# Kernel optimization log

Measured on AMD Instinct MI355X. Metric: run time of the kernel, lower is better.

The kernel has to match this reference:

```python
import jax, jax.numpy as jnp
import numpy as np

LOG_SIG_MIN, LOG_SIG_MAX = -20.0, 2.0
BN_EPS = 1e-5

def leaky_relu(x):
    return jnp.where(x >= 0, x, 0.01 * x)

def setup_inputs() -> dict:
    key = jax.random.key(0)
    ks = jax.random.split(key, 12)
    E, B, N, H, A = 8, 16384, 64, 512, 8  # encoders, batch, nagents, hidden, heads
    d = H // A
    f32 = jnp.float32
    inp = {}
    inp['states'] = jax.random.normal(ks[0], (E, B, N), dtype=f32)
    inp['pre_actions'] = jax.random.normal(ks[1], (B, H), dtype=f32)
    inp['W_enc'] = jax.random.normal(ks[2], (E, N, H), dtype=f32) / np.sqrt(N)
    inp['b_enc'] = jnp.zeros((E, H), dtype=f32)
    inp['W_pre'] = jax.random.normal(ks[3], (H, H), dtype=f32) / np.sqrt(H)
    inp['b_pre'] = jnp.zeros((H,), dtype=f32)
    inp['Wk'] = jax.random.normal(ks[4], (A, H, d), dtype=f32) / np.sqrt(H)
    inp['Wsel'] = jax.random.normal(ks[5], (A, H, d), dtype=f32) / np.sqrt(H)
    inp['Wv'] = jax.random.normal(ks[6], (A, H, d), dtype=f32) / np.sqrt(H)
    inp['bv'] = jnp.zeros((A, d), dtype=f32)
    inp['W_actor'] = jax.random.normal(ks[7], (H, H), dtype=f32) / np.sqrt(H)
    inp['b_actor'] = jnp.zeros((H,), dtype=f32)
    inp['W_mean'] = jax.random.normal(ks[8], (H, N), dtype=f32) / np.sqrt(H)
    inp['b_mean'] = jnp.zeros((N,), dtype=f32)
    inp['W_logstd'] = jax.random.normal(ks[9], (H, N), dtype=f32) / np.sqrt(H)
    inp['b_logstd'] = jnp.zeros((N,), dtype=f32)
    return inp

def reference(states, pre_actions, W_enc, b_enc, W_pre, b_pre, Wk, Wsel, Wv, bv,
              W_actor, b_actor, W_mean, b_mean, W_logstd, b_logstd):
    # states: [E, B, N]; per-encoder BatchNorm1d (training-mode batch stats, no affine)
    mu = states.mean(axis=1, keepdims=True)                      # [E,1,N]
    var = states.var(axis=1, keepdims=True)                      # biased var, as torch BN
    s_norm = (states - mu) * jax.lax.rsqrt(var + BN_EPS)
    # per-encoder Linear + LeakyReLU -> encodings [E, B, H]
    encs = leaky_relu(jnp.einsum('ebn,enh->ebh', s_norm, W_enc) + b_enc[:, None, :])
    # per-head keys/values over all encoders: [A, E, B, d]
    keys = jnp.einsum('ebh,ahd->aebd', encs, Wk)
    vals = leaky_relu(jnp.einsum('ebh,ahd->aebd', encs, Wv) + bv[:, None, None, :])
    # selector from encoded previous actions: [A, B, d]
    pre = leaky_relu(pre_actions @ W_pre + b_pre)                 # [B, H]
    sel = jnp.einsum('bh,ahd->abd', pre, Wsel)
    d = keys.shape[-1]
    logits = jnp.einsum('abd,aebd->abe', sel, keys)               # [A, B, E]
    w = jax.nn.softmax(logits / np.sqrt(d), axis=-1)
    attn = jnp.einsum('aebd,abe->abd', vals, w)                   # [A, B, d]
    B = attn.shape[1]
    actor_in = jnp.transpose(attn, (1, 0, 2)).reshape(B, -1)      # [B, A*d] head-concat
    x = jax.nn.relu(actor_in @ W_actor + b_actor)
    mean = x @ W_mean + b_mean
    log_std = jnp.clip(x @ W_logstd + b_logstd, LOG_SIG_MIN, LOG_SIG_MAX)
    return mean, log_std, actor_in
```

## Files before the change

kernel.cpp:

```cpp
#include <hip/hip_runtime.h>
#include <hip/hip_bf16.h>
#include <stdint.h>

#define E_ 8
#define B_ 16384
#define N_ 64
#define H_ 512
#define A_ 8
#define D_ 64

typedef __hip_bfloat16 bf16;
typedef __attribute__((ext_vector_type(8))) short s8v;
typedef __attribute__((ext_vector_type(4))) float f4v;

__device__ __forceinline__ float bf2f(bf16 v) { return __bfloat162float(v); }
__device__ __forceinline__ bf16 f2bf(float v) { return __float2bfloat16(v); }
__device__ __forceinline__ short f2bfs(float v) {
    bf16 b = f2bf(v); short s; __builtin_memcpy(&s, &b, 2); return s;
}
__device__ __forceinline__ float bfs2f(short s) {
    bf16 b; __builtin_memcpy(&b, &s, 2); return bf2f(b);
}

__device__ __forceinline__ void async_load16(const void* g, void* l) {
    __builtin_amdgcn_global_load_lds(
        (const __attribute__((address_space(1))) void*)g,
        (__attribute__((address_space(3))) void*)l, 16, 0, 0);
}

__device__ __forceinline__ int swz_off(int row, int krow) {
    return row * 64 + (((krow >> 3) ^ (row & 7)) << 3);
}

template <int CB>
__device__ __forceinline__ void xcd_map(int x, int nBm, int& bm, int& bn) {
    if ((nBm & 7) == 0) {
        int j = x & 7, s = x >> 3;
        bn = s & ((1 << CB) - 1);
        bm = ((s >> CB) << 3) | j;
    } else {
        bm = x >> CB;
        bn = x & ((1 << CB) - 1);
    }
}

__global__ __launch_bounds__(256) void bnPart(const float* __restrict__ states,
                                              float* __restrict__ part,
                                              bf16* __restrict__ sbf) {
    int blk = blockIdx.x;
    int e = blk >> 6, sl = blk & 63;
    int tid = threadIdx.x, n = tid & 63, rg = tid >> 6;
    const long rowBase = (long)e * B_ + (long)sl * 256;
    const float* base = states + rowBase * 64;
    float s1 = 0.f, s2 = 0.f;
    for (int i = 0; i < 64; ++i) {
        float v = base[(rg + i * 4) * 64 + n];
        s1 += v; s2 += v * v;
        sbf[(rowBase + rg + i * 4) * 64 + n] = f2bf(v);
    }
    __shared__ float sh[2][4][64];
    sh[0][rg][n] = s1; sh[1][rg][n] = s2;
    __syncthreads();
    if (tid < 64) {
        float t1 = sh[0][0][n] + sh[0][1][n] + sh[0][2][n] + sh[0][3][n];
        float t2 = sh[1][0][n] + sh[1][1][n] + sh[1][2][n] + sh[1][3][n];
        part[((long)blk * 64 + n) * 2 + 0] = t1;
        part[((long)blk * 64 + n) * 2 + 1] = t2;
    }
}

__global__ void bnFin(const float* __restrict__ part, float* __restrict__ mu_rstd) {
    int idx = blockIdx.x * blockDim.x + threadIdx.x;
    if (idx >= E_ * 64) return;
    int e = idx >> 6, n = idx & 63;
    float s1 = 0.f, s2 = 0.f;
    for (int sl = 0; sl < 64; ++sl) {
        s1 += part[(((long)e * 64 + sl) * 64 + n) * 2 + 0];
        s2 += part[(((long)e * 64 + sl) * 64 + n) * 2 + 1];
    }
    float mu = s1 / (float)B_;
    float var = s2 / (float)B_ - mu * mu;
    mu_rstd[idx * 2 + 0] = mu;
    mu_rstd[idx * 2 + 1] = rsqrtf(var + 1e-5f);
}

__global__ void foldEnc(const float* __restrict__ W_enc, const float* __restrict__ b_enc,
                        const float* __restrict__ mu_rstd,
                        bf16* __restrict__ WencfT, float* __restrict__ bencf) {
    int idx = blockIdx.x * 256 + threadIdx.x;
    int e = idx >> 9, h = idx & 511;
    float acc = b_enc[e * 512 + h];
    for (int n = 0; n < 64; ++n) {
        float mu = mu_rstd[(e * 64 + n) * 2 + 0];
        float rs = mu_rstd[(e * 64 + n) * 2 + 1];
        float w = W_enc[((long)e * 64 + n) * 512 + h];
        WencfT[((long)e * 512 + h) * 64 + n] = f2bf(w * rs);
        acc -= mu * rs * w;
    }
    bencf[e * 512 + h] = acc;
}

__global__ __launch_bounds__(256) void packAll(
    const float* __restrict__ W_pre, const float* __restrict__ W_actor,
    const float* __restrict__ Wsel, const float* __restrict__ Wk,
    const float* __restrict__ Wv, const float* __restrict__ wm,
    const float* __restrict__ wl, const float* __restrict__ pre_actions,
    bf16* __restrict__ WpreT, bf16* __restrict__ WactorT, bf16* __restrict__ WselT,
    bf16* __restrict__ WkvaT, bf16* __restrict__ WmlT, bf16* __restrict__ pa_bf) {
    int bx = blockIdx.x, tid = threadIdx.x;
    if (bx < 2048) {
        const float* in = (bx < 1024) ? W_pre : W_actor;
        bf16* out = (bx < 1024) ? WpreT : WactorT;
        int idx = (bx & 1023) * 256 + tid;
        int n = idx >> 9, k = idx & 511;
        out[idx] = f2bf(in[k * 512 + n]);
    } else if (bx < 3072) {
        int idx = (bx - 2048) * 256 + tid;
        int n = idx >> 9, h = idx & 511;
        int a = n >> 6, dd = n & 63;
        WselT[idx] = f2bf(Wsel[((long)a * 512 + h) * 64 + dd]);
    } else if (bx < 5120) {
        int idx = (bx - 3072) * 256 + tid;
        int n = idx >> 9, h = idx & 511;
        int a = n >> 7, j = n & 127;
        const float* src = (j < 64) ? Wk : Wv;
        WkvaT[idx] = f2bf(src[((long)a * 512 + h) * 64 + (j & 63)]);
    } else if (bx < 5376) {
        int idx = (bx - 5120) * 256 + tid;
        int n = idx >> 9, k = idx & 511;
        float v = (n < 64) ? wm[k * 64 + n] : wl[k * 64 + (n - 64)];
        WmlT[idx] = f2bf(v);
    } else {
        int i = (bx - 5376) * 256 + tid;
        float4 v = ((const float4*)pre_actions)[i];
        bf16 o[4] = {f2bf(v.x), f2bf(v.y), f2bf(v.z), f2bf(v.w)};
        __builtin_memcpy(pa_bf + (long)i * 4, o, 8);
    }
}

template <int ACT, int OUTF, bool HAS_BIAS, int CB>
__global__ __launch_bounds__(256) void gemm_bt(
    const bf16* __restrict__ Ag, const bf16* __restrict__ Bg,
    const float* __restrict__ bias, const float* __restrict__ bias2,
    void* __restrict__ out, void* __restrict__ out2,
    int M, int Nn, int K, long sA, long sB, long sBias, long sO) {
    const int tid = threadIdx.x, lane = tid & 63, wid = tid >> 6;
    const int wm = wid >> 1, wn = wid & 1;
    int bm, bn;
    xcd_map<CB>(blockIdx.x, gridDim.x >> CB, bm, bn);
    const int bz = blockIdx.z;
    const bf16* Aptr = Ag + (long)bz * sA + (long)bm * 128 * K;
    const bf16* Bptr = Bg + (long)bz * sB + (long)bn * 128 * K;

    __shared__ __align__(16) short sAl[128 * 64];
    __shared__ __align__(16) short sBl[128 * 64];

    const int srow = lane >> 3;
    const int scol = (((lane & 7) ^ srow) << 3);

    f4v acc[4][4];
#pragma unroll
    for (int i = 0; i < 4; ++i)
#pragma unroll
        for (int j = 0; j < 4; ++j) acc[i][j] = f4v{0.f, 0.f, 0.f, 0.f};

    for (int k0 = 0; k0 < K; k0 += 64) {
#pragma unroll
        for (int i = 0; i < 4; ++i) {
            int r = (wid * 4 + i) * 8 + srow;
            async_load16(Aptr + (long)r * K + k0 + scol, (char*)sAl + (wid * 4 + i) * 1024);
            async_load16(Bptr + (long)r * K + k0 + scol, (char*)sBl + (wid * 4 + i) * 1024);
        }
        __syncthreads();
#pragma unroll
        for (int kk = 0; kk < 64; kk += 32) {
            int krow = kk + (lane >> 4) * 8;
            s8v af[4], bfr[4];
#pragma unroll
            for (int mi = 0; mi < 4; ++mi)
                af[mi] = *(const s8v*)(sAl + swz_off(wm * 64 + mi * 16 + (lane & 15), krow));
#pragma unroll
            for (int ni = 0; ni < 4; ++ni)
                bfr[ni] = *(const s8v*)(sBl + swz_off(wn * 64 + ni * 16 + (lane & 15), krow));
#pragma unroll
            for (int mi = 0; mi < 4; ++mi)
#pragma unroll
                for (int ni = 0; ni < 4; ++ni)
                    acc[mi][ni] = __builtin_amdgcn_mfma_f32_16x16x32_bf16(
                        af[mi], bfr[ni], acc[mi][ni], 0, 0, 0);
        }
        __syncthreads();
    }

    long m0 = (long)bm * 128 + wm * 64;
    long n0 = (long)bn * 128 + wn * 64;
#pragma unroll
    for (int mi = 0; mi < 4; ++mi)
#pragma unroll
        for (int ni = 0; ni < 4; ++ni)
#pragma unroll
            for (int r = 0; r < 4; ++r) {
                long gm = m0 + mi * 16 + (lane >> 4) * 4 + r;
                long gn = n0 + ni * 16 + (lane & 15);
                float v = acc[mi][ni][r];
                if constexpr (HAS_BIAS) v += bias[sBias * bz + gn];
                if constexpr (ACT == 1) v = (v >= 0.f) ? v : 0.01f * v;
                if constexpr (ACT == 2) v = fmaxf(v, 0.f);
                if constexpr (OUTF == 0) {
                    ((bf16*)out)[(long)bz * sO + gm * Nn + gn] = f2bf(v);
                } else if constexpr (OUTF == 1) {
                    ((float*)out)[(long)bz * sO + gm * Nn + gn] = v;
                } else if constexpr (OUTF == 2) {
                    if (gn < 64) {
                        ((float*)out)[gm * 64 + gn] = v + bias[gn];
                    } else {
                        float w = v + bias2[gn - 64];
                        w = fminf(fmaxf(w, -20.f), 2.f);
                        ((float*)out2)[gm * 64 + (gn - 64)] = w;
                    }
                } else {
                    ((bf16*)out)[(gm * E_ + bz) * 512 + gn] = f2bf(v);
                }
            }
}

__global__ __launch_bounds__(256) void kv_attn(
    const bf16* __restrict__ Ag, const bf16* __restrict__ Bg,
    const float* __restrict__ bv, const float* __restrict__ sel,
    float* __restrict__ actor_f32, bf16* __restrict__ attn_bf, int b0) {
    const int tid = threadIdx.x, lane = tid & 63, wid = tid >> 6;
    const int wm = wid >> 1, wn = wid & 1;
    int bm, a;
    xcd_map<3>(blockIdx.x, gridDim.x >> 3, bm, a);
    const bf16* Aptr = Ag + (long)bm * 128 * 512;
    const bf16* Bptr = Bg + (long)a * 128 * 512;

    __shared__ __align__(16) short smem[17408];
    __shared__ float lgs[128];
    short* sAl = smem;
    short* sBl = smem + 128 * 64;

    const long bgBase = (long)b0 + (long)bm * 16;

    s8v bselH[2], bselL[2];
#pragma unroll
    for (int kk = 0; kk < 2; ++kk) {
        const float* sp = sel + (bgBase + (lane & 15)) * 512 + a * 64 + kk * 32 + (lane >> 4) * 8;
#pragma unroll
        for (int j = 0; j < 8; ++j) {
            float s = sp[j] * 0.125f;
            short h = f2bfs(s);
            bselH[kk][j] = h;
            bselL[kk][j] = f2bfs(s - bfs2f(h));
        }
    }

    const int srow = lane >> 3;
    const int scol = (((lane & 7) ^ srow) << 3);

    f4v acc[4][4];
#pragma unroll
    for (int i = 0; i < 4; ++i)
#pragma unroll
        for (int j = 0; j < 4; ++j) acc[i][j] = f4v{0.f, 0.f, 0.f, 0.f};

    for (int k0 = 0; k0 < 512; k0 += 64) {
#pragma unroll
        for (int i = 0; i < 4; ++i) {
            int r = (wid * 4 + i) * 8 + srow;
            async_load16(Aptr + (long)r * 512 + k0 + scol, (char*)sAl + (wid * 4 + i) * 1024);
            async_load16(Bptr + (long)r * 512 + k0 + scol, (char*)sBl + (wid * 4 + i) * 1024);
        }
        __syncthreads();
#pragma unroll
        for (int kk = 0; kk < 64; kk += 32) {
            int krow = kk + (lane >> 4) * 8;
            s8v af[4], bfr[4];
#pragma unroll
            for (int mi = 0; mi < 4; ++mi)
                af[mi] = *(const s8v*)(sAl + swz_off(wm * 64 + mi * 16 + (lane & 15), krow));
#pragma unroll
            for (int ni = 0; ni < 4; ++ni)
                bfr[ni] = *(const s8v*)(sBl + swz_off(wn * 64 + ni * 16 + (lane & 15), krow));
#pragma unroll
            for (int mi = 0; mi < 4; ++mi)
#pragma unroll
                for (int ni = 0; ni < 4; ++ni)
                    acc[mi][ni] = __builtin_amdgcn_mfma_f32_16x16x32_bf16(
                        af[mi], bfr[ni], acc[mi][ni], 0, 0, 0);
        }
        __syncthreads();
    }

    short* keysC = smem;
    short* vT    = smem + 9216;
    const int quad = lane >> 4, cl = lane & 15;
#pragma unroll
    for (int mi = 0; mi < 4; ++mi)
#pragma unroll
        for (int ni = 0; ni < 4; ++ni)
#pragma unroll
            for (int r = 0; r < 4; ++r) {
                int row = wm * 64 + mi * 16 + quad * 4 + r;
                float v = acc[mi][ni][r];
                if (wn == 0) {
                    keysC[row * 72 + ni * 16 + cl] = f2bfs(v);
                } else {
                    int d = ni * 16 + cl;
                    v += bv[a * 64 + d];
                    v = (v >= 0.f) ? v : 0.01f * v;
                    vT[d * 128 + (row ^ ((d & 15) << 3))] = f2bfs(v);
                }
            }
    __syncthreads();

    {
        f4v lgacc[2] = {f4v{0.f, 0.f, 0.f, 0.f}, f4v{0.f, 0.f, 0.f, 0.f}};
#pragma unroll
        for (int kk = 0; kk < 2; ++kk) {
#pragma unroll
            for (int mi = 0; mi < 2; ++mi) {
                s8v af = *(const s8v*)(keysC + (wid * 32 + mi * 16 + cl) * 72 +
                                       kk * 32 + quad * 8);
                lgacc[mi] = __builtin_amdgcn_mfma_f32_16x16x32_bf16(
                    af, bselH[kk], lgacc[mi], 0, 0, 0);
                lgacc[mi] = __builtin_amdgcn_mfma_f32_16x16x32_bf16(
                    af, bselL[kk], lgacc[mi], 0, 0, 0);
            }
        }
#pragma unroll
        for (int mi = 0; mi < 2; ++mi)
#pragma unroll
            for (int r = 0; r < 4; ++r) {
                int grow = wid * 32 + mi * 16 + quad * 4 + r;
                if (cl == (grow >> 3)) lgs[grow] = lgacc[mi][r];
            }
    }
    __syncthreads();

#pragma unroll
    for (int t = 0; t < 4; ++t) {
        int lb = wid * 4 + t, row0 = lb * 8;
        s8v vvv = *(const s8v*)(vT + lane * 128 + (row0 ^ ((lane & 15) << 3)));
        float lg[8], vv[8];
#pragma unroll
        for (int e = 0; e < 8; ++e) {
            vv[e] = bfs2f(vvv[e]);
            lg[e] = lgs[row0 + e];
        }
        float mx = lg[0];
#pragma unroll
        for (int e = 1; e < 8; ++e) mx = fmaxf(mx, lg[e]);
        float ssum = 0.f, w[8];
#pragma unroll
        for (int e = 0; e < 8; ++e) { w[e] = __expf(lg[e] - mx); ssum += w[e]; }
        float inv = 1.f / ssum;
        float at = 0.f;
#pragma unroll
        for (int e = 0; e < 8; ++e) at += vv[e] * (w[e] * inv);
        long o = (bgBase + lb) * 512 + a * 64 + lane;
        actor_f32[o] = at;
        attn_bf[o] = f2bf(at);
    }
}

extern "C" void kernel_launch(void* const* d_in, const int* in_sizes, int n_in,
                              void* d_out, int out_size, void* d_ws, size_t ws_size,
                              hipStream_t stream) {
    (void)in_sizes; (void)n_in; (void)out_size;
    const float* states      = (const float*)d_in[0];
    const float* pre_actions = (const float*)d_in[1];
    const float* W_enc       = (const float*)d_in[2];
    const float* b_enc       = (const float*)d_in[3];
    const float* W_pre       = (const float*)d_in[4];
    const float* b_pre       = (const float*)d_in[5];
    const float* Wk          = (const float*)d_in[6];
    const float* Wsel        = (const float*)d_in[7];
    const float* Wv          = (const float*)d_in[8];
    const float* bv          = (const float*)d_in[9];
    const float* W_actor     = (const float*)d_in[10];
    const float* b_actor     = (const float*)d_in[11];
    const float* W_mean      = (const float*)d_in[12];
    const float* b_mean      = (const float*)d_in[13];
    const float* W_logstd    = (const float*)d_in[14];
    const float* b_logstd    = (const float*)d_in[15];

    char* ws = (char*)d_ws;
    size_t off = 0;
    auto alloc = [&](size_t bytes) -> void* {
        void* p = ws + off;
        off = (off + bytes + 255) & ~(size_t)255;
        return p;
    };
    float* mu_rstd = (float*)alloc((size_t)E_ * 64 * 2 * 4);
    float* bnpart  = (float*)alloc((size_t)E_ * 64 * 64 * 2 * 4);
    bf16* WencfT   = (bf16*)alloc((size_t)E_ * 512 * 64 * 2);
    float* bencf   = (float*)alloc((size_t)E_ * 512 * 4);
    bf16* WpreT    = (bf16*)alloc((size_t)512 * 512 * 2);
    bf16* WselT    = (bf16*)alloc((size_t)512 * 512 * 2);
    bf16* WkvaT    = (bf16*)alloc((size_t)1024 * 512 * 2);
    bf16* WactorT  = (bf16*)alloc((size_t)512 * 512 * 2);
    bf16* WmlT     = (bf16*)alloc((size_t)128 * 512 * 2);
    bf16* pa_bf    = (bf16*)alloc((size_t)B_ * 512 * 2);
    bf16* p_pre    = (bf16*)alloc((size_t)B_ * 512 * 2);
    float* p_sel   = (float*)alloc((size_t)B_ * 512 * 4);
    bf16* s_bf     = (bf16*)alloc((size_t)E_ * B_ * 64 * 2);
    bf16* p_attn = pa_bf;
    bf16* p_x    = p_pre;

    size_t remaining = (ws_size > off) ? ws_size - off : 0;
    int Bc = B_;
    while (Bc > 128 && (size_t)Bc * 8192 + 4096 > remaining) Bc >>= 1;
    const int NC = B_ / Bc;
    bf16* c_encs = (bf16*)alloc((size_t)E_ * Bc * 512 * 2);

    packAll<<<13568, 256, 0, stream>>>(W_pre, W_actor, Wsel, Wk, Wv, W_mean, W_logstd,
                                       pre_actions, WpreT, WactorT, WselT, WkvaT, WmlT,
                                       pa_bf);
    bnPart<<<512, 256, 0, stream>>>(states, bnpart, s_bf);
    bnFin<<<2, 256, 0, stream>>>(bnpart, mu_rstd);
    foldEnc<<<16, 256, 0, stream>>>(W_enc, b_enc, mu_rstd, WencfT, bencf);

    gemm_bt<1, 0, true, 2><<<dim3((B_ / 128) << 2, 1, 1), 256, 0, stream>>>(
        pa_bf, WpreT, b_pre, nullptr, p_pre, nullptr, B_, 512, 512, 0, 0, 0, 0);
    gemm_bt<0, 1, false, 2><<<dim3((B_ / 128) << 2, 1, 1), 256, 0, stream>>>(
        p_pre, WselT, nullptr, nullptr, p_sel, nullptr, B_, 512, 512, 0, 0, 0, 0);

    float* actor_out = (float*)d_out + 2L * B_ * 64;
    for (int c = 0; c < NC; ++c) {
        int b0 = c * Bc;
        gemm_bt<1, 4, true, 2><<<dim3((Bc / 128) << 2, 1, E_), 256, 0, stream>>>(
            s_bf + (long)b0 * 64, WencfT, bencf, nullptr, c_encs, nullptr, Bc, 512, 64,
            (long)B_ * 64, (long)512 * 64, 512, 0);
        kv_attn<<<dim3((Bc / 16) * 8, 1, 1), 256, 0, stream>>>(
            c_encs, WkvaT, bv, p_sel, actor_out, p_attn, b0);
    }

    gemm_bt<2, 0, true, 2><<<dim3((B_ / 128) << 2, 1, 1), 256, 0, stream>>>(
        p_attn, WactorT, b_actor, nullptr, p_x, nullptr, B_, 512, 512, 0, 0, 0, 0);
    gemm_bt<0, 2, false, 0><<<dim3(B_ / 128, 1, 1), 256, 0, stream>>>(
        p_x, WmlT, b_mean, b_logstd, (float*)d_out, (float*)d_out + (long)B_ * 64,
        B_, 128, 512, 0, 0, 0, 0);
}
```

Measured before the change: 573.5 us.

## Double-buffer the A tile in kv_attn to overlap its global loads with MFMA

The kv_attn GEMM main loop now double-buffers the encoding (A) tile in shared memory. The next A tile is prefetched asynchronously while MFMAs run on the current one. The weight (B) tile stays single-buffered: it is loaded after each compute step and followed by an extra barrier, so its latency is still exposed. Shared memory grows, which may lower occupancy, and the epilogue now reuses the split buffers for keys and the transposed values.

```diff
diff --git a/kernel.cpp b/kernel.cpp
--- a/kernel.cpp
+++ b/kernel.cpp
@@ -235,10 +235,9 @@
     const bf16* Aptr = Ag + (long)bm * 128 * 512;
     const bf16* Bptr = Bg + (long)a * 128 * 512;
 
-    __shared__ __align__(16) short smem[17408];
+    __shared__ __align__(16) short sA[2 * 8192];
+    __shared__ __align__(16) short sB[8192];
     __shared__ float lgs[128];
-    short* sAl = smem;
-    short* sBl = smem + 128 * 64;
 
     const long bgBase = (long)b0 + (long)bm * 16;
 
@@ -258,30 +257,46 @@
     const int srow = lane >> 3;
     const int scol = (((lane & 7) ^ srow) << 3);
 
-    f4v acc[4][4];
-#pragma unroll
-    for (int i = 0; i < 4; ++i)
-#pragma unroll
-        for (int j = 0; j < 4; ++j) acc[i][j] = f4v{0.f, 0.f, 0.f, 0.f};
-
-    for (int k0 = 0; k0 < 512; k0 += 64) {
+    auto stageA = [&](int kt, int buf) {
 #pragma unroll
         for (int i = 0; i < 4; ++i) {
             int r = (wid * 4 + i) * 8 + srow;
-            async_load16(Aptr + (long)r * 512 + k0 + scol, (char*)sAl + (wid * 4 + i) * 1024);
-            async_load16(Bptr + (long)r * 512 + k0 + scol, (char*)sBl + (wid * 4 + i) * 1024);
-        }
-        __syncthreads();
+            async_load16(Aptr + (long)r * 512 + kt * 64 + scol,
+                         (char*)(sA + buf * 8192) + (wid * 4 + i) * 1024);
+        }
+    };
+    auto stageB = [&](int kt) {
+#pragma unroll
+        for (int i = 0; i < 4; ++i) {
+            int r = (wid * 4 + i) * 8 + srow;
+            async_load16(Bptr + (long)r * 512 + kt * 64 + scol,
+                         (char*)sB + (wid * 4 + i) * 1024);
+        }
+    };
+
+    f4v acc[4][4];
+#pragma unroll
+    for (int i = 0; i < 4; ++i)
+#pragma unroll
+        for (int j = 0; j < 4; ++j) acc[i][j] = f4v{0.f, 0.f, 0.f, 0.f};
+
+    stageA(0, 0);
+    stageB(0);
+    __syncthreads();
+    int cur = 0;
+    for (int t = 0; t < 8; ++t) {
+        if (t < 7) stageA(t + 1, cur ^ 1);
+        const short* sAc = sA + cur * 8192;
 #pragma unroll
         for (int kk = 0; kk < 64; kk += 32) {
             int krow = kk + (lane >> 4) * 8;
             s8v af[4], bfr[4];
 #pragma unroll
             for (int mi = 0; mi < 4; ++mi)
-                af[mi] = *(const s8v*)(sAl + swz_off(wm * 64 + mi * 16 + (lane & 15), krow));
+                af[mi] = *(const s8v*)(sAc + swz_off(wm * 64 + mi * 16 + (lane & 15), krow));
 #pragma unroll
             for (int ni = 0; ni < 4; ++ni)
-                bfr[ni] = *(const s8v*)(sBl + swz_off(wn * 64 + ni * 16 + (lane & 15), krow));
+                bfr[ni] = *(const s8v*)(sB + swz_off(wn * 64 + ni * 16 + (lane & 15), krow));
 #pragma unroll
             for (int mi = 0; mi < 4; ++mi)
 #pragma unroll
@@ -290,10 +305,15 @@
                         af[mi], bfr[ni], acc[mi][ni], 0, 0, 0);
         }
         __syncthreads();
-    }
-
-    short* keysC = smem;
-    short* vT    = smem + 9216;
+        if (t < 7) {
+            stageB(t + 1);
+            __syncthreads();
+        }
+        cur ^= 1;
+    }
+
+    short* keysC = sA;
+    short* vT    = sB;
     const int quad = lane >> 4, cl = lane & 15;
 #pragma unroll
     for (int mi = 0; mi < 4; ++mi)
```

Result: faster. 556.7 us (-2.9%).

## Double-buffer kv_attn K-loop and widen block to 512 threads

Applied to the files above, without the earlier changes.

The kv_attn kernel now runs with 512 threads (8 waves) per block, each wave computing half as many M rows. The LDS staging is double-buffered so the next K tile is async-loaded while MFMAs run on the current one, and the per-iteration barrier count drops. The selector load moves after the main loop to reduce register pressure. LDS per block grows to 64KB, which may limit blocks per CU.

```diff
diff --git a/kernel.cpp b/kernel.cpp
--- a/kernel.cpp
+++ b/kernel.cpp
@@ -224,7 +224,7 @@
             }
 }
 
-__global__ __launch_bounds__(256) void kv_attn(
+__global__ __launch_bounds__(512, 4) void kv_attn(
     const bf16* __restrict__ Ag, const bf16* __restrict__ Bg,
     const float* __restrict__ bv, const float* __restrict__ sel,
     float* __restrict__ actor_f32, bf16* __restrict__ attn_bf, int b0) {
@@ -235,73 +235,69 @@
     const bf16* Aptr = Ag + (long)bm * 128 * 512;
     const bf16* Bptr = Bg + (long)a * 128 * 512;
 
-    __shared__ __align__(16) short smem[17408];
+    __shared__ __align__(16) short smem[32768];
     __shared__ float lgs[128];
-    short* sAl = smem;
-    short* sBl = smem + 128 * 64;
 
     const long bgBase = (long)b0 + (long)bm * 16;
-
-    s8v bselH[2], bselL[2];
-#pragma unroll
-    for (int kk = 0; kk < 2; ++kk) {
-        const float* sp = sel + (bgBase + (lane & 15)) * 512 + a * 64 + kk * 32 + (lane >> 4) * 8;
-#pragma unroll
-        for (int j = 0; j < 8; ++j) {
-            float s = sp[j] * 0.125f;
-            short h = f2bfs(s);
-            bselH[kk][j] = h;
-            bselL[kk][j] = f2bfs(s - bfs2f(h));
-        }
-    }
 
     const int srow = lane >> 3;
     const int scol = (((lane & 7) ^ srow) << 3);
 
-    f4v acc[4][4];
-#pragma unroll
-    for (int i = 0; i < 4; ++i)
+    auto stage = [&](int kt, int buf) {
+#pragma unroll
+        for (int i = 0; i < 2; ++i) {
+            int r = (wid * 2 + i) * 8 + srow;
+            async_load16(Aptr + (long)r * 512 + kt * 64 + scol,
+                         (char*)(smem + buf * 8192) + (wid * 2 + i) * 1024);
+            async_load16(Bptr + (long)r * 512 + kt * 64 + scol,
+                         (char*)(smem + 16384 + buf * 8192) + (wid * 2 + i) * 1024);
+        }
+    };
+
+    f4v acc[2][4];
+#pragma unroll
+    for (int i = 0; i < 2; ++i)
 #pragma unroll
         for (int j = 0; j < 4; ++j) acc[i][j] = f4v{0.f, 0.f, 0.f, 0.f};
 
-    for (int k0 = 0; k0 < 512; k0 += 64) {
-#pragma unroll
-        for (int i = 0; i < 4; ++i) {
-            int r = (wid * 4 + i) * 8 + srow;
-            async_load16(Aptr + (long)r * 512 + k0 + scol, (char*)sAl + (wid * 4 + i) * 1024);
-            async_load16(Bptr + (long)r * 512 + k0 + scol, (char*)sBl + (wid * 4 + i) * 1024);
-        }
-        __syncthreads();
+    stage(0, 0);
+    __syncthreads();
+    int cur = 0;
+    for (int t = 0; t < 8; ++t) {
+        if (t < 7) stage(t + 1, cur ^ 1);
+        const short* sAc = smem + cur * 8192;
+        const short* sBc = smem + 16384 + cur * 8192;
 #pragma unroll
         for (int kk = 0; kk < 64; kk += 32) {
             int krow = kk + (lane >> 4) * 8;
-            s8v af[4], bfr[4];
-#pragma unroll
-            for (int mi = 0; mi < 4; ++mi)
-                af[mi] = *(const s8v*)(sAl + swz_off(wm * 64 + mi * 16 + (lane & 15), krow));
+            s8v af[2], bfr[4];
+#pragma unroll
+            for (int mi = 0; mi < 2; ++mi)
+                af[mi] = *(const s8v*)(sAc + swz_off(wm * 32 + mi * 16 + (lane & 15), krow));
 #pragma unroll
             for (int ni = 0; ni < 4; ++ni)
-                bfr[ni] = *(const s8v*)(sBl + swz_off(wn * 64 + ni * 16 + (lane & 15), krow));
-#pragma unroll
-            for (int mi = 0; mi < 4; ++mi)
+                bfr[ni] = *(const s8v*)(sBc + swz_off(wn * 64 + ni * 16 + (lane & 15), krow));
+#pragma unroll
+            for (int mi = 0; mi < 2; ++mi)
 #pragma unroll
                 for (int ni = 0; ni < 4; ++ni)
                     acc[mi][ni] = __builtin_amdgcn_mfma_f32_16x16x32_bf16(
                         af[mi], bfr[ni], acc[mi][ni], 0, 0, 0);
         }
         __syncthreads();
+        cur ^= 1;
     }
 
     short* keysC = smem;
     short* vT    = smem + 9216;
     const int quad = lane >> 4, cl = lane & 15;
 #pragma unroll
-    for (int mi = 0; mi < 4; ++mi)
+    for (int mi = 0; mi < 2; ++mi)
 #pragma unroll
         for (int ni = 0; ni < 4; ++ni)
 #pragma unroll
             for (int r = 0; r < 4; ++r) {
-                int row = wm * 64 + mi * 16 + quad * 4 + r;
+                int row = wm * 32 + mi * 16 + quad * 4 + r;
                 float v = acc[mi][ni][r];
                 if (wn == 0) {
                     keysC[row * 72 + ni * 16 + cl] = f2bfs(v);
@@ -312,35 +308,40 @@
                     vT[d * 128 + (row ^ ((d & 15) << 3))] = f2bfs(v);
                 }
             }
+
+    s8v bselH[2], bselL[2];
+#pragma unroll
+    for (int kk = 0; kk < 2; ++kk) {
+        const float* sp = sel + (bgBase + cl) * 512 + a * 64 + kk * 32 + quad * 8;
+#pragma unroll
+        for (int j = 0; j < 8; ++j) {
+            float s = sp[j] * 0.125f;
+            short h = f2bfs(s);
+            bselH[kk][j] = h;
+            bselL[kk][j] = f2bfs(s - bfs2f(h));
+        }
+    }
     __syncthreads();
 
     {
-        f4v lgacc[2] = {f4v{0.f, 0.f, 0.f, 0.f}, f4v{0.f, 0.f, 0.f, 0.f}};
+        f4v lgacc = f4v{0.f, 0.f, 0.f, 0.f};
 #pragma unroll
         for (int kk = 0; kk < 2; ++kk) {
-#pragma unroll
-            for (int mi = 0; mi < 2; ++mi) {
-                s8v af = *(const s8v*)(keysC + (wid * 32 + mi * 16 + cl) * 72 +
-                                       kk * 32 + quad * 8);
-                lgacc[mi] = __builtin_amdgcn_mfma_f32_16x16x32_bf16(
-                    af, bselH[kk], lgacc[mi], 0, 0, 0);
-                lgacc[mi] = __builtin_amdgcn_mfma_f32_16x16x32_bf16(
-                    af, bselL[kk], lgacc[mi], 0, 0, 0);
-            }
-        }
-#pragma unroll
-        for (int mi = 0; mi < 2; ++mi)
-#pragma unroll
-            for (int r = 0; r < 4; ++r) {
-                int grow = wid * 32 + mi * 16 + quad * 4 + r;
-                if (cl == (grow >> 3)) lgs[grow] = lgacc[mi][r];
-            }
+            s8v af = *(const s8v*)(keysC + (wid * 16 + cl) * 72 + kk * 32 + quad * 8);
+            lgacc = __builtin_amdgcn_mfma_f32_16x16x32_bf16(af, bselH[kk], lgacc, 0, 0, 0);
+            lgacc = __builtin_amdgcn_mfma_f32_16x16x32_bf16(af, bselL[kk], lgacc, 0, 0, 0);
+        }
+#pragma unroll
+        for (int r = 0; r < 4; ++r) {
+            int grow = wid * 16 + quad * 4 + r;
+            if (cl == (grow >> 3)) lgs[grow] = lgacc[r];
+        }
     }
     __syncthreads();
 
 #pragma unroll
-    for (int t = 0; t < 4; ++t) {
-        int lb = wid * 4 + t, row0 = lb * 8;
+    for (int t = 0; t < 2; ++t) {
+        int lb = wid * 2 + t, row0 = lb * 8;
         s8v vvv = *(const s8v*)(vT + lane * 128 + (row0 ^ ((lane & 15) << 3)));
         float lg[8], vv[8];
 #pragma unroll
@@ -432,7 +433,7 @@
         gemm_bt<1, 4, true, 2><<<dim3((Bc / 128) << 2, 1, E_), 256, 0, stream>>>(
             s_bf + (long)b0 * 64, WencfT, bencf, nullptr, c_encs, nullptr, Bc, 512, 64,
             (long)B_ * 64, (long)512 * 64, 512, 0);
-        kv_attn<<<dim3((Bc / 16) * 8, 1, 1), 256, 0, stream>>>(
+        kv_attn<<<dim3((Bc / 16) * 8, 1, 1), 512, 0, stream>>>(
             c_encs, WkvaT, bv, p_sel, actor_out, p_attn, b0);
     }
 
```

Result: faster. 503.8 us (-12.2%).
